# Kernel tuning notes

Hardware: AMD Instinct MI355X
Metric: run time of the kernel (lower is better)

## Reference

```python
import jax, jax.numpy as jnp
import numpy as np


def gcn_conv(x, src, dst, W, b, num_nodes):
    # PyG GCNConv: add self-loops, symmetric deg^-1/2 normalization, scatter-add.
    h = x @ W                                    # [N, out]
    loops = jnp.arange(num_nodes, dtype=src.dtype)
    s = jnp.concatenate([src, loops])            # [E+N]
    d = jnp.concatenate([dst, loops])            # [E+N]
    deg = jax.ops.segment_sum(jnp.ones_like(d, dtype=h.dtype), d, num_segments=num_nodes)
    dinv = jnp.where(deg > 0, jax.lax.rsqrt(deg), 0.0)
    norm = dinv[s] * dinv[d]                     # [E+N]
    msgs = h[s] * norm[:, None]                  # gather + scale  [E+N, out]
    out = jax.ops.segment_sum(msgs, d, num_segments=num_nodes)
    return out + b


NUM_GRAPHS = 512


def setup_inputs() -> dict:
    key = jax.random.key(0)
    ks = jax.random.split(key, 12)
    N, E, F = 50000, 400000, 128
    x = jax.random.normal(ks[0], (N, F), dtype=jnp.float32)
    edge_index = jax.random.randint(ks[1], (2, E), 0, N, dtype=jnp.int64)
    batch = jnp.sort(jax.random.randint(ks[2], (N,), 0, NUM_GRAPHS, dtype=jnp.int64))
    def lin(k, fi, fo):
        return jax.random.normal(k, (fi, fo), dtype=jnp.float32) * (1.0 / np.sqrt(fi))
    return {
        "x": x, "edge_index": edge_index, "batch": batch,
        "W1": lin(ks[3], F, 512), "b1": jnp.zeros((512,), jnp.float32),
        "W2": lin(ks[4], 512, 256), "b2": jnp.zeros((256,), jnp.float32),
        "W3": lin(ks[5], 256, 128), "b3": jnp.zeros((128,), jnp.float32),
        "W4": lin(ks[6], 128, 32), "b4": jnp.zeros((32,), jnp.float32),
        "W5": lin(ks[7], 32, 10), "b5": jnp.zeros((10,), jnp.float32),
    }


def reference(x, edge_index, batch, W1, b1, W2, b2, W3, b3, W4, b4, W5, b5):
    N = x.shape[0]
    src, dst = edge_index[0], edge_index[1]
    h = gcn_conv(x, src, dst, W1, b1, N)
    h = jax.nn.leaky_relu(h, negative_slope=0.01)
    h = gcn_conv(h, src, dst, W2, b2, N)          # [N, 256]
    embs = jax.ops.segment_max(h, batch, num_segments=NUM_GRAPHS)  # [G, 256]
    z = ((h @ W3 + b3) @ W4 + b4) @ W5 + b5       # [N, 10]
    out = jax.ops.segment_max(z, batch, num_segments=NUM_GRAPHS)   # [G, 10]
    return (out, embs)
```

## Files before the change

kernel.cpp:

```cpp
#include <hip/hip_runtime.h>
#include <math.h>

#define DIV_UP(a,b) (((a)+(b)-1)/(b))

typedef __attribute__((ext_vector_type(8))) short bf16x8;
typedef __attribute__((ext_vector_type(4))) float f32x4;

__device__ inline unsigned short f2b(float x) {
    unsigned int u = __float_as_uint(x);
    u += 0x7fffu + ((u >> 16) & 1u);
    return (unsigned short)(u >> 16);
}

__device__ inline void cvt8(uint4 v, float* a) {
    a[0] = __uint_as_float(v.x << 16); a[1] = __uint_as_float(v.x & 0xffff0000u);
    a[2] = __uint_as_float(v.y << 16); a[3] = __uint_as_float(v.y & 0xffff0000u);
    a[4] = __uint_as_float(v.z << 16); a[5] = __uint_as_float(v.z & 0xffff0000u);
    a[6] = __uint_as_float(v.w << 16); a[7] = __uint_as_float(v.w & 0xffff0000u);
}

__device__ inline void gl16(void* lds, const void* g) {
    __builtin_amdgcn_global_load_lds(
        (const __attribute__((address_space(1))) void*)g,
        (__attribute__((address_space(3))) void*)lds, 16, 0, 0);
}

__global__ void k_zero_i(int* p, int n) {
    int i = blockIdx.x * blockDim.x + threadIdx.x;
    if (i < n) p[i] = 0;
}

__global__ void k_hist(const int* __restrict__ dst, int* __restrict__ hist, int E) {
    int i = blockIdx.x * blockDim.x + threadIdx.x;
    if (i < E) atomicAdd(&hist[dst[i]], 1);
}

__global__ __launch_bounds__(256) void k_scan_bsum(const int* __restrict__ hist,
                                                   int* __restrict__ bsum, int N) {
    __shared__ int red[256];
    int t = threadIdx.x;
    int base = blockIdx.x * 1024 + t * 4;
    int s = 0;
    if (base + 3 < N) {
        int4 v = *(const int4*)&hist[base];
        s = v.x + v.y + v.z + v.w;
    } else {
        for (int j = 0; j < 4; ++j) if (base + j < N) s += hist[base + j];
    }
    red[t] = s;
    __syncthreads();
    for (int off = 128; off >= 1; off >>= 1) {
        if (t < off) red[t] += red[t + off];
        __syncthreads();
    }
    if (t == 0) bsum[blockIdx.x] = red[0];
}

__global__ __launch_bounds__(1024) void k_scan_boff(const int* __restrict__ bsum,
        int* __restrict__ boff, int* __restrict__ row_off, int NB, int N) {
    __shared__ int s[1024];
    int t = threadIdx.x;
    int v = (t < NB) ? bsum[t] : 0;
    s[t] = v;
    __syncthreads();
    for (int off = 1; off < 1024; off <<= 1) {
        int u = (t >= off) ? s[t - off] : 0;
        __syncthreads();
        s[t] += u;
        __syncthreads();
    }
    if (t < NB) boff[t] = s[t] - v;
    if (t == NB - 1) row_off[N] = s[t];
}

__global__ __launch_bounds__(256) void k_scan_apply(const int* __restrict__ hist,
        const int* __restrict__ boff, int* __restrict__ row_off,
        float* __restrict__ dinv, int N) {
    __shared__ int s[256];
    int t = threadIdx.x;
    int base = blockIdx.x * 1024 + t * 4;
    int v[4];
    int loc = 0;
#pragma unroll
    for (int j = 0; j < 4; ++j) { v[j] = (base + j < N) ? hist[base + j] : 0; loc += v[j]; }
    s[t] = loc;
    __syncthreads();
    for (int off = 1; off < 256; off <<= 1) {
        int u = (t >= off) ? s[t - off] : 0;
        __syncthreads();
        s[t] += u;
        __syncthreads();
    }
    int run = boff[blockIdx.x] + s[t] - loc;
#pragma unroll
    for (int j = 0; j < 4; ++j) {
        if (base + j < N) {
            row_off[base + j] = run;
            dinv[base + j] = rsqrtf((float)(v[j] + 1));
        }
        run += v[j];
    }
}

__global__ void k_bin(const int* __restrict__ src, const int* __restrict__ dst,
                      const int* __restrict__ row_off, int* __restrict__ cursor,
                      const float* __restrict__ dinv,
                      int* __restrict__ csr_src, float* __restrict__ csr_w, int E) {
    int i = blockIdx.x * blockDim.x + threadIdx.x;
    if (i >= E) return;
    int d = dst[i], s = src[i];
    int pos = row_off[d] + atomicAdd(&cursor[d], 1);
    csr_src[pos] = s;
    csr_w[pos] = dinv[s] * dinv[d];
}

__global__ __launch_bounds__(256) void k_pre(
        const float* __restrict__ W3, const float* __restrict__ W4,
        const float* __restrict__ W5, const float* __restrict__ b3,
        const float* __restrict__ b4, const float* __restrict__ b5,
        float* __restrict__ WcT, float* __restrict__ bc,
        const int* __restrict__ batch, int* __restrict__ bounds, int N, int G, int nb,
        const float* __restrict__ x, unsigned short* __restrict__ xb, int n4,
        const float* __restrict__ W1, unsigned short* __restrict__ w1t, int K1, int N1,
        const float* __restrict__ W2, unsigned short* __restrict__ w2t, int K2, int N2) {
    int b = blockIdx.x;
    int t = threadIdx.x;
    if (b < 11) {
        int c = b;
        if (c < 10) {
            __shared__ float Tc[128];
            if (t < 128) {
                float s = 0.f;
#pragma unroll 8
                for (int k = 0; k < 32; ++k) s = fmaf(W4[t * 32 + k], W5[k * 10 + c], s);
                Tc[t] = s;
            }
            __syncthreads();
            float s = 0.f;
            const float* w3r = &W3[t * 128];
#pragma unroll 8
            for (int j = 0; j < 128; ++j) s = fmaf(w3r[j], Tc[j], s);
            WcT[c * 256 + t] = s;
        } else {
            __shared__ float v[32];
            if (t < 32) {
                float s = b4[t];
                for (int j = 0; j < 128; ++j) s = fmaf(b3[j], W4[j * 32 + t], s);
                v[t] = s;
            }
            __syncthreads();
            if (t < 10) {
                float s = b5[t];
                for (int k = 0; k < 32; ++k) s = fmaf(v[k], W5[k * 10 + t], s);
                bc[t] = s;
            }
        }
        return;
    }
    if (b < 11 + nb) {
        int g = (b - 11) * 256 + t;
        if (g > G) return;
        int lo = 0, hi = N;
        while (lo < hi) { int mid = (lo + hi) >> 1; if (batch[mid] < g) lo = mid + 1; else hi = mid; }
        bounds[g] = lo;
        return;
    }
    int i = (b - 11 - nb) * 256 + t;
    if (i < n4) {
        float4 v = ((const float4*)x)[i];
        ushort4 o;
        o.x = f2b(v.x); o.y = f2b(v.y); o.z = f2b(v.z); o.w = f2b(v.w);
        ((ushort4*)xb)[i] = o;
        return;
    }
    i -= n4;
    if (i < K1 * N1) {
        int k = i / N1, n = i % N1;
        w1t[(size_t)n * K1 + k] = f2b(W1[i]);
        return;
    }
    i -= K1 * N1;
    if (i < K2 * N2) {
        int k = i / N2, n = i % N2;
        w2t[(size_t)n * K2 + k] = f2b(W2[i]);
    }
}

template <int F>
__global__ __launch_bounds__(256) void k_gather_b(const unsigned short* __restrict__ H,
        const int* __restrict__ row_off, const int* __restrict__ csr_src,
        const float* __restrict__ csr_w, const float* __restrict__ dinv,
        const float* __restrict__ bias, unsigned short* __restrict__ outb, int N) {
    const int LPN = F / 8;
    const int NPB = 256 / LPN;
    int node = blockIdx.x * NPB + threadIdx.x / LPN;
    if (node >= N) return;
    int f = (threadIdx.x % LPN) * 8;
    const unsigned short* Hf = H + f;
    float sc = dinv[node]; sc *= sc;
    float a[8];
    cvt8(*(const uint4*)&Hf[(size_t)node * F], a);
#pragma unroll
    for (int j = 0; j < 8; ++j) a[j] *= sc;
    if (bias) {
#pragma unroll
        for (int j = 0; j < 8; ++j) a[j] += bias[f + j];
    }
    int e0 = row_off[node], e1 = row_off[node + 1];
    int e = e0;
    for (; e + 4 <= e1; e += 4) {
        int s0 = csr_src[e + 0], s1 = csr_src[e + 1];
        int s2 = csr_src[e + 2], s3 = csr_src[e + 3];
        uint4 v0 = *(const uint4*)&Hf[(size_t)s0 * F];
        uint4 v1 = *(const uint4*)&Hf[(size_t)s1 * F];
        uint4 v2 = *(const uint4*)&Hf[(size_t)s2 * F];
        uint4 v3 = *(const uint4*)&Hf[(size_t)s3 * F];
        float w0 = csr_w[e + 0], w1 = csr_w[e + 1];
        float w2 = csr_w[e + 2], w3 = csr_w[e + 3];
        float b0[8], b1[8], b2[8], b3[8];
        cvt8(v0, b0); cvt8(v1, b1); cvt8(v2, b2); cvt8(v3, b3);
#pragma unroll
        for (int j = 0; j < 8; ++j) {
            a[j] = fmaf(w0, b0[j], a[j]);
            a[j] = fmaf(w1, b1[j], a[j]);
            a[j] = fmaf(w2, b2[j], a[j]);
            a[j] = fmaf(w3, b3[j], a[j]);
        }
    }
    for (; e < e1; ++e) {
        int s = csr_src[e];
        float w = csr_w[e];
        float b[8];
        cvt8(*(const uint4*)&Hf[(size_t)s * F], b);
#pragma unroll
        for (int j = 0; j < 8; ++j) a[j] = fmaf(w, b[j], a[j]);
    }
    uint4 o;
    o.x = (unsigned)f2b(a[0]) | ((unsigned)f2b(a[1]) << 16);
    o.y = (unsigned)f2b(a[2]) | ((unsigned)f2b(a[3]) << 16);
    o.z = (unsigned)f2b(a[4]) | ((unsigned)f2b(a[5]) << 16);
    o.w = (unsigned)f2b(a[6]) | ((unsigned)f2b(a[7]) << 16);
    *(uint4*)&outb[(size_t)node * F + f] = o;
}

template <int OUT_BF16, int ACT>
__global__ __launch_bounds__(512) void k_gemm_mfma256(const unsigned short* __restrict__ A,
        const unsigned short* __restrict__ Bt, const float* __restrict__ bias,
        void* __restrict__ Cout, int M, int K, int NC) {
    __shared__ __align__(16) unsigned short As[128][64];
    __shared__ __align__(16) unsigned short Bs[256][64];
    int tid = threadIdx.x;
    int wave = tid >> 6, lane = tid & 63;
    int row0 = blockIdx.y * 128, col0 = blockIdx.x * 256;
    int wr = (wave >> 2) * 64, wc = (wave & 3) * 64;
    f32x4 acc[4][4] = {};
    int lr = lane & 15;
    int lg = lane >> 4;
    int sw = ((lane & 7) ^ (lane >> 3)) << 3;
    int ch0 = (lg ^ (lr & 7)) << 3;
    int ch1 = ch0 ^ (4 << 3);

    for (int k0 = 0; k0 < K; k0 += 64) {
#pragma unroll
        for (int c = 0; c < 2; ++c) {
            int rl = c * 64 + wave * 8 + (lane >> 3);
            int gr = min(row0 + rl, M - 1);
            gl16(&As[c * 64 + wave * 8][0], &A[(size_t)gr * K + k0 + sw]);
        }
#pragma unroll
        for (int c = 0; c < 4; ++c) {
            int rl = c * 64 + wave * 8 + (lane >> 3);
            gl16(&Bs[c * 64 + wave * 8][0], &Bt[(size_t)(col0 + rl) * K + k0 + sw]);
        }
        __syncthreads();
        bf16x8 af[2][4], bv[2][4];
#pragma unroll
        for (int i = 0; i < 4; ++i) {
            int ra = wr + i * 16 + lr;
            int rb = wc + i * 16 + lr;
            af[0][i] = *(const bf16x8*)&As[ra][ch0];
            af[1][i] = *(const bf16x8*)&As[ra][ch1];
            bv[0][i] = *(const bf16x8*)&Bs[rb][ch0];
            bv[1][i] = *(const bf16x8*)&Bs[rb][ch1];
        }
#pragma unroll
        for (int s = 0; s < 2; ++s)
#pragma unroll
            for (int i = 0; i < 4; ++i)
#pragma unroll
                for (int j = 0; j < 4; ++j)
                    acc[i][j] = __builtin_amdgcn_mfma_f32_16x16x32_bf16(bv[s][j], af[s][i], acc[i][j], 0, 0, 0);
        __syncthreads();
    }

    int q4 = lg * 4;
    float4 bb[4];
#pragma unroll
    for (int j = 0; j < 4; ++j)
        bb[j] = bias ? *(const float4*)&bias[col0 + wc + j * 16 + q4]
                     : make_float4(0.f, 0.f, 0.f, 0.f);
#pragma unroll
    for (int i = 0; i < 4; ++i) {
        int row = row0 + wr + i * 16 + lr;
        if (row >= M) continue;
#pragma unroll
        for (int j = 0; j < 4; ++j) {
            int c0 = col0 + wc + j * 16 + q4;
            float4 v;
            v.x = acc[i][j][0] + bb[j].x;
            v.y = acc[i][j][1] + bb[j].y;
            v.z = acc[i][j][2] + bb[j].z;
            v.w = acc[i][j][3] + bb[j].w;
            if (ACT) {
                v.x = (v.x >= 0.f) ? v.x : 0.01f * v.x;
                v.y = (v.y >= 0.f) ? v.y : 0.01f * v.y;
                v.z = (v.z >= 0.f) ? v.z : 0.01f * v.z;
                v.w = (v.w >= 0.f) ? v.w : 0.01f * v.w;
            }
            if (OUT_BF16) {
                uint2 o;
                o.x = (unsigned)f2b(v.x) | ((unsigned)f2b(v.y) << 16);
                o.y = (unsigned)f2b(v.z) | ((unsigned)f2b(v.w) << 16);
                *(uint2*)&((unsigned short*)Cout)[(size_t)row * NC + c0] = o;
            } else {
                *(float4*)&((float*)Cout)[(size_t)row * NC + c0] = v;
            }
        }
    }
}

__global__ __launch_bounds__(320) void k_head_segmax(const unsigned short* __restrict__ H,
        const float* __restrict__ WcT, const float* __restrict__ bc,
        const int* __restrict__ bounds, float* __restrict__ out,
        float* __restrict__ out_emb) {
    __shared__ __align__(16) float Ws[10][260];
    __shared__ float bs[10];
    __shared__ float red[320];
    int t = threadIdx.x;
    for (int i = t; i < 2560; i += 320) Ws[i / 256][i % 256] = WcT[i];
    if (t < 10) bs[t] = bc[t];
    __syncthreads();
    int g = blockIdx.x;
    int s = bounds[g], e = bounds[g + 1];
    int col = t % 10, rs = t / 10;
    float m = -INFINITY;
    for (int r = s + rs; r < e; r += 32) {
        const unsigned short* hr = &H[(size_t)r * 256];
        float acc = bs[col];
#pragma unroll 4
        for (int k = 0; k < 256; k += 8) {
            float h[8];
            cvt8(*(const uint4*)&hr[k], h);
            float4 wa = *(const float4*)&Ws[col][k];
            float4 wb = *(const float4*)&Ws[col][k + 4];
            acc = fmaf(h[0], wa.x, acc);
            acc = fmaf(h[1], wa.y, acc);
            acc = fmaf(h[2], wa.z, acc);
            acc = fmaf(h[3], wa.w, acc);
            acc = fmaf(h[4], wb.x, acc);
            acc = fmaf(h[5], wb.y, acc);
            acc = fmaf(h[6], wb.z, acc);
            acc = fmaf(h[7], wb.w, acc);
        }
        m = fmaxf(m, acc);
    }
    red[t] = m;
    __syncthreads();
    for (int step = 16; step >= 1; step >>= 1) {
        if (rs < step) red[rs * 10 + col] = fmaxf(red[rs * 10 + col], red[(rs + step) * 10 + col]);
        __syncthreads();
    }
    if (rs == 0) out[(size_t)g * 10 + col] = red[col];
    if (t < 256) {
        float mm = -INFINITY;
        for (int r = s; r < e; ++r)
            mm = fmaxf(mm, __uint_as_float(((unsigned)H[(size_t)r * 256 + t]) << 16));
        out_emb[(size_t)g * 256 + t] = mm;
    }
}

extern "C" void kernel_launch(void* const* d_in, const int* in_sizes, int n_in,
                              void* d_out, int out_size, void* d_ws, size_t ws_size,
                              hipStream_t stream) {
    const float* x  = (const float*)d_in[0];
    const int* ei   = (const int*)d_in[1];
    const int* batch= (const int*)d_in[2];
    const float* W1 = (const float*)d_in[3];
    const float* b1 = (const float*)d_in[4];
    const float* W2 = (const float*)d_in[5];
    const float* b2 = (const float*)d_in[6];
    const float* W3 = (const float*)d_in[7];
    const float* b3 = (const float*)d_in[8];
    const float* W4 = (const float*)d_in[9];
    const float* b4 = (const float*)d_in[10];
    const float* W5 = (const float*)d_in[11];
    const float* b5 = (const float*)d_in[12];

    const int N  = in_sizes[2];
    const int F  = in_sizes[0] / N;
    const int E  = in_sizes[1] / 2;
    const int C1 = in_sizes[4];
    const int C2 = in_sizes[6];
    const int C5 = in_sizes[12];
    const int G  = out_size / (C2 + C5);
    const int NB = DIV_UP(N, 1024);

    const int* srcp = ei;
    const int* dstp = ei + E;

    uintptr_t p = (uintptr_t)d_ws;
    auto carve = [&](size_t bytes) {
        uintptr_t r = p;
        p += (bytes + 255) & ~(size_t)255;
        return (void*)r;
    };
    int* hist    = (int*)carve(sizeof(int) * N);
    int* cursor  = (int*)carve(sizeof(int) * N);
    int* row_off = (int*)carve(sizeof(int) * (N + 1));
    int* bounds  = (int*)carve(sizeof(int) * (G + 1));
    int* bsum    = (int*)carve(sizeof(int) * NB);
    int* boff    = (int*)carve(sizeof(int) * NB);
    int* csr_src = (int*)carve(sizeof(int) * E);
    float* csr_w = (float*)carve(sizeof(float) * E);
    float* dinv  = (float*)carve(sizeof(float) * N);
    float* wct   = (float*)carve(sizeof(float) * C2 * C5);
    float* bcv   = (float*)carve(sizeof(float) * C5);
    unsigned short* w1t = (unsigned short*)carve(sizeof(short) * F * C1);
    unsigned short* w2t = (unsigned short*)carve(sizeof(short) * C1 * C2);
    unsigned short* xb    = (unsigned short*)carve(sizeof(short) * (size_t)N * F);
    unsigned short* aggxb = (unsigned short*)carve(sizeof(short) * (size_t)N * F);
    unsigned short* h1b   = (unsigned short*)carve(sizeof(short) * (size_t)N * C1);
    unsigned short* t2b   = (unsigned short*)carve(sizeof(short) * (size_t)N * C2);
    unsigned short* h2b   = (unsigned short*)carve(sizeof(short) * (size_t)N * C2);

    float* out     = (float*)d_out;
    float* out_emb = out + (size_t)G * C5;

    int zspan = (int)(((sizeof(int) * N + 255) & ~(size_t)255) / 4) + N;
    k_zero_i<<<DIV_UP(zspan, 256), 256, 0, stream>>>(hist, zspan);
    k_hist<<<DIV_UP(E, 256), 256, 0, stream>>>(dstp, hist, E);
    k_scan_bsum<<<NB, 256, 0, stream>>>(hist, bsum, N);
    k_scan_boff<<<1, 1024, 0, stream>>>(bsum, boff, row_off, NB, N);
    k_scan_apply<<<NB, 256, 0, stream>>>(hist, boff, row_off, dinv, N);
    k_bin<<<DIV_UP(E, 256), 256, 0, stream>>>(srcp, dstp, row_off, cursor, dinv,
                                              csr_src, csr_w, E);

    int n4 = N * F / 4;
    int nb_bounds = DIV_UP(G + 1, 256);
    int prep_total = n4 + F * C1 + C1 * C2;
    int pre_blocks = 11 + nb_bounds + DIV_UP(prep_total, 256);
    k_pre<<<pre_blocks, 256, 0, stream>>>(W3, W4, W5, b3, b4, b5, wct, bcv,
                                          batch, bounds, N, G, nb_bounds,
                                          x, xb, n4, W1, w1t, F, C1, W2, w2t, C1, C2);

    k_gather_b<128><<<DIV_UP(N, 16), 256, 0, stream>>>(
        xb, row_off, csr_src, csr_w, dinv, nullptr, aggxb, N);
    dim3 g1(C1 / 256, DIV_UP(N, 128));
    k_gemm_mfma256<1, 1><<<g1, 512, 0, stream>>>(aggxb, w1t, b1, h1b, N, F, C1);

    dim3 g2(C2 / 256, DIV_UP(N, 128));
    k_gemm_mfma256<1, 0><<<g2, 512, 0, stream>>>(h1b, w2t, nullptr, t2b, N, C1, C2);
    k_gather_b<256><<<DIV_UP(N, 8), 256, 0, stream>>>(
        t2b, row_off, csr_src, csr_w, dinv, b2, h2b, N);

    k_head_segmax<<<G, 320, 0, stream>>>(h2b, wct, bcv, bounds, out, out_emb);
}
```

Measured before the change: 286.4 us.

## Fuse CSR build and preprocessing into one cooperative grid-synced kernel

Replaces the zero, histogram, three-pass scan, binning and preprocessing launches with a single cooperative kernel that separates the phases with grid-wide syncs, removing several launch gaps and small-kernel tails. The gather kernel also gains an 8-edge unrolled loop so more neighbor-row loads are in flight at once. The risks are grid.sync costs, a fixed 256x1024 grid that may not suit every phase, and higher register pressure in the gather.

```diff
diff --git a/kernel.cpp b/kernel.cpp
--- a/kernel.cpp
+++ b/kernel.cpp
@@ -1,5 +1,8 @@
 #include <hip/hip_runtime.h>
+#include <hip/hip_cooperative_groups.h>
 #include <math.h>
+
+namespace cg = cooperative_groups;
 
 #define DIV_UP(a,b) (((a)+(b)-1)/(b))
 
@@ -25,164 +28,139 @@
         (__attribute__((address_space(3))) void*)lds, 16, 0, 0);
 }
 
-__global__ void k_zero_i(int* p, int n) {
-    int i = blockIdx.x * blockDim.x + threadIdx.x;
-    if (i < n) p[i] = 0;
-}
-
-__global__ void k_hist(const int* __restrict__ dst, int* __restrict__ hist, int E) {
-    int i = blockIdx.x * blockDim.x + threadIdx.x;
-    if (i < E) atomicAdd(&hist[dst[i]], 1);
-}
-
-__global__ __launch_bounds__(256) void k_scan_bsum(const int* __restrict__ hist,
-                                                   int* __restrict__ bsum, int N) {
-    __shared__ int red[256];
-    int t = threadIdx.x;
-    int base = blockIdx.x * 1024 + t * 4;
-    int s = 0;
-    if (base + 3 < N) {
-        int4 v = *(const int4*)&hist[base];
-        s = v.x + v.y + v.z + v.w;
-    } else {
-        for (int j = 0; j < 4; ++j) if (base + j < N) s += hist[base + j];
-    }
-    red[t] = s;
-    __syncthreads();
-    for (int off = 128; off >= 1; off >>= 1) {
-        if (t < off) red[t] += red[t + off];
-        __syncthreads();
-    }
-    if (t == 0) bsum[blockIdx.x] = red[0];
-}
-
-__global__ __launch_bounds__(1024) void k_scan_boff(const int* __restrict__ bsum,
-        int* __restrict__ boff, int* __restrict__ row_off, int NB, int N) {
-    __shared__ int s[1024];
-    int t = threadIdx.x;
-    int v = (t < NB) ? bsum[t] : 0;
-    s[t] = v;
-    __syncthreads();
-    for (int off = 1; off < 1024; off <<= 1) {
-        int u = (t >= off) ? s[t - off] : 0;
-        __syncthreads();
-        s[t] += u;
-        __syncthreads();
-    }
-    if (t < NB) boff[t] = s[t] - v;
-    if (t == NB - 1) row_off[N] = s[t];
-}
-
-__global__ __launch_bounds__(256) void k_scan_apply(const int* __restrict__ hist,
-        const int* __restrict__ boff, int* __restrict__ row_off,
-        float* __restrict__ dinv, int N) {
-    __shared__ int s[256];
-    int t = threadIdx.x;
-    int base = blockIdx.x * 1024 + t * 4;
-    int v[4];
-    int loc = 0;
-#pragma unroll
-    for (int j = 0; j < 4; ++j) { v[j] = (base + j < N) ? hist[base + j] : 0; loc += v[j]; }
-    s[t] = loc;
-    __syncthreads();
-    for (int off = 1; off < 256; off <<= 1) {
-        int u = (t >= off) ? s[t - off] : 0;
-        __syncthreads();
-        s[t] += u;
-        __syncthreads();
-    }
-    int run = boff[blockIdx.x] + s[t] - loc;
-#pragma unroll
-    for (int j = 0; j < 4; ++j) {
-        if (base + j < N) {
-            row_off[base + j] = run;
-            dinv[base + j] = rsqrtf((float)(v[j] + 1));
-        }
-        run += v[j];
-    }
-}
-
-__global__ void k_bin(const int* __restrict__ src, const int* __restrict__ dst,
-                      const int* __restrict__ row_off, int* __restrict__ cursor,
-                      const float* __restrict__ dinv,
-                      int* __restrict__ csr_src, float* __restrict__ csr_w, int E) {
-    int i = blockIdx.x * blockDim.x + threadIdx.x;
-    if (i >= E) return;
-    int d = dst[i], s = src[i];
-    int pos = row_off[d] + atomicAdd(&cursor[d], 1);
-    csr_src[pos] = s;
-    csr_w[pos] = dinv[s] * dinv[d];
-}
-
-__global__ __launch_bounds__(256) void k_pre(
+__global__ __launch_bounds__(1024) void k_build(
+        const int* __restrict__ src, const int* __restrict__ dst, int E,
+        int* __restrict__ hist, int* __restrict__ cursor, int* __restrict__ bsum,
+        int* __restrict__ row_off, float* __restrict__ dinv, int N,
+        int* __restrict__ csr_src, float* __restrict__ csr_w,
+        const int* __restrict__ batch, int* __restrict__ bounds, int G,
         const float* __restrict__ W3, const float* __restrict__ W4,
         const float* __restrict__ W5, const float* __restrict__ b3,
         const float* __restrict__ b4, const float* __restrict__ b5,
         float* __restrict__ WcT, float* __restrict__ bc,
-        const int* __restrict__ batch, int* __restrict__ bounds, int N, int G, int nb,
         const float* __restrict__ x, unsigned short* __restrict__ xb, int n4,
         const float* __restrict__ W1, unsigned short* __restrict__ w1t, int K1, int N1,
         const float* __restrict__ W2, unsigned short* __restrict__ w2t, int K2, int N2) {
-    int b = blockIdx.x;
-    int t = threadIdx.x;
-    if (b < 11) {
-        int c = b;
-        if (c < 10) {
-            __shared__ float Tc[128];
-            if (t < 128) {
-                float s = 0.f;
-#pragma unroll 8
-                for (int k = 0; k < 32; ++k) s = fmaf(W4[t * 32 + k], W5[k * 10 + c], s);
-                Tc[t] = s;
-            }
-            __syncthreads();
-            float s = 0.f;
-            const float* w3r = &W3[t * 128];
-#pragma unroll 8
-            for (int j = 0; j < 128; ++j) s = fmaf(w3r[j], Tc[j], s);
-            WcT[c * 256 + t] = s;
-        } else {
-            __shared__ float v[32];
-            if (t < 32) {
-                float s = b4[t];
-                for (int j = 0; j < 128; ++j) s = fmaf(b3[j], W4[j * 32 + t], s);
-                v[t] = s;
-            }
-            __syncthreads();
-            if (t < 10) {
-                float s = b5[t];
-                for (int k = 0; k < 32; ++k) s = fmaf(v[k], W5[k * 10 + t], s);
-                bc[t] = s;
-            }
-        }
-        return;
-    }
-    if (b < 11 + nb) {
-        int g = (b - 11) * 256 + t;
-        if (g > G) return;
-        int lo = 0, hi = N;
-        while (lo < hi) { int mid = (lo + hi) >> 1; if (batch[mid] < g) lo = mid + 1; else hi = mid; }
-        bounds[g] = lo;
-        return;
-    }
-    int i = (b - 11 - nb) * 256 + t;
-    if (i < n4) {
+    cg::grid_group grid = cg::this_grid();
+    __shared__ float shf[256];
+    __shared__ int ssc[1024];
+    const int nb = gridDim.x;
+    const int b = blockIdx.x, t = threadIdx.x;
+    const int gtid = b * blockDim.x + t;
+    const int gsz = nb * blockDim.x;
+
+    for (int i = gtid; i < N; i += gsz) { hist[i] = 0; cursor[i] = 0; }
+    for (int i = gtid; i < n4; i += gsz) {
         float4 v = ((const float4*)x)[i];
         ushort4 o;
         o.x = f2b(v.x); o.y = f2b(v.y); o.z = f2b(v.z); o.w = f2b(v.w);
         ((ushort4*)xb)[i] = o;
-        return;
-    }
-    i -= n4;
-    if (i < K1 * N1) {
+    }
+    for (int i = gtid; i < K1 * N1; i += gsz) {
         int k = i / N1, n = i % N1;
         w1t[(size_t)n * K1 + k] = f2b(W1[i]);
-        return;
-    }
-    i -= K1 * N1;
-    if (i < K2 * N2) {
+    }
+    for (int i = gtid; i < K2 * N2; i += gsz) {
         int k = i / N2, n = i % N2;
         w2t[(size_t)n * K2 + k] = f2b(W2[i]);
+    }
+    for (int g = gtid; g <= G; g += gsz) {
+        int lo = 0, hi = N;
+        while (lo < hi) { int mid = (lo + hi) >> 1; if (batch[mid] < g) lo = mid + 1; else hi = mid; }
+        bounds[g] = lo;
+    }
+    if (b < 10) {
+        int c = b;
+        if (t < 128) {
+            float s = 0.f;
+#pragma unroll 8
+            for (int k = 0; k < 32; ++k) s = fmaf(W4[t * 32 + k], W5[k * 10 + c], s);
+            shf[t] = s;
+        }
+        __syncthreads();
+        if (t < 256) {
+            float s = 0.f;
+            const float* w3r = &W3[t * 128];
+#pragma unroll 8
+            for (int j = 0; j < 128; ++j) s = fmaf(w3r[j], shf[j], s);
+            WcT[c * 256 + t] = s;
+        }
+        __syncthreads();
+    } else if (b == 10) {
+        if (t < 32) {
+            float s = b4[t];
+            for (int j = 0; j < 128; ++j) s = fmaf(b3[j], W4[j * 32 + t], s);
+            shf[t] = s;
+        }
+        __syncthreads();
+        if (t < 10) {
+            float s = b5[t];
+            for (int k = 0; k < 32; ++k) s = fmaf(shf[k], W5[k * 10 + t], s);
+            bc[t] = s;
+        }
+        __syncthreads();
+    }
+    grid.sync();
+
+    for (int i = gtid; i < E; i += gsz) atomicAdd(&hist[dst[i]], 1);
+    grid.sync();
+
+    const int chunk = DIV_UP(N, nb);
+    const int beg = b * chunk;
+    const int end = min(beg + chunk, N);
+    {
+        int s = 0;
+        for (int i = beg + t; i < end; i += 1024) s += hist[i];
+        ssc[t] = s;
+        __syncthreads();
+        for (int off = 512; off >= 1; off >>= 1) {
+            if (t < off) ssc[t] += ssc[t + off];
+            __syncthreads();
+        }
+        if (t == 0) bsum[b] = ssc[0];
+    }
+    grid.sync();
+
+    {
+        int v = (t < nb) ? bsum[t] : 0;
+        ssc[t] = v;
+        __syncthreads();
+        for (int off = 1; off < 1024; off <<= 1) {
+            int u = (t >= off) ? ssc[t - off] : 0;
+            __syncthreads();
+            ssc[t] += u;
+            __syncthreads();
+        }
+        int boffv = (b == 0) ? 0 : ssc[b - 1];
+        __syncthreads();
+        int carry = boffv;
+        for (int s0 = beg; s0 < end; s0 += 1024) {
+            int i = s0 + t;
+            int v2 = (i < end) ? hist[i] : 0;
+            ssc[t] = v2;
+            __syncthreads();
+            for (int off = 1; off < 1024; off <<= 1) {
+                int u = (t >= off) ? ssc[t - off] : 0;
+                __syncthreads();
+                ssc[t] += u;
+                __syncthreads();
+            }
+            if (i < end) {
+                row_off[i] = carry + ssc[t] - v2;
+                dinv[i] = rsqrtf((float)(v2 + 1));
+            }
+            carry += ssc[1023];
+            __syncthreads();
+        }
+        if (b == nb - 1 && t == 0) row_off[N] = carry;
+    }
+    grid.sync();
+
+    for (int i = gtid; i < E; i += gsz) {
+        int d = dst[i], s = src[i];
+        int pos = row_off[d] + atomicAdd(&cursor[d], 1);
+        csr_src[pos] = s;
+        csr_w[pos] = dinv[s] * dinv[d];
     }
 }
 
@@ -208,6 +186,24 @@
     }
     int e0 = row_off[node], e1 = row_off[node + 1];
     int e = e0;
+    for (; e + 8 <= e1; e += 8) {
+        int ss[8];
+        uint4 vv[8];
+        float ww[8];
+#pragma unroll
+        for (int q = 0; q < 8; ++q) ss[q] = csr_src[e + q];
+#pragma unroll
+        for (int q = 0; q < 8; ++q) vv[q] = *(const uint4*)&Hf[(size_t)ss[q] * F];
+#pragma unroll
+        for (int q = 0; q < 8; ++q) ww[q] = csr_w[e + q];
+#pragma unroll
+        for (int q = 0; q < 8; ++q) {
+            float bb[8];
+            cvt8(vv[q], bb);
+#pragma unroll
+            for (int j = 0; j < 8; ++j) a[j] = fmaf(ww[q], bb[j], a[j]);
+        }
+    }
     for (; e + 4 <= e1; e += 4) {
         int s0 = csr_src[e + 0], s1 = csr_src[e + 1];
         int s2 = csr_src[e + 2], s3 = csr_src[e + 3];
@@ -398,12 +394,11 @@
 
     const int N  = in_sizes[2];
     const int F  = in_sizes[0] / N;
-    const int E  = in_sizes[1] / 2;
+    int E        = in_sizes[1] / 2;
     const int C1 = in_sizes[4];
     const int C2 = in_sizes[6];
     const int C5 = in_sizes[12];
     const int G  = out_size / (C2 + C5);
-    const int NB = DIV_UP(N, 1024);
 
     const int* srcp = ei;
     const int* dstp = ei + E;
@@ -418,8 +413,7 @@
     int* cursor  = (int*)carve(sizeof(int) * N);
     int* row_off = (int*)carve(sizeof(int) * (N + 1));
     int* bounds  = (int*)carve(sizeof(int) * (G + 1));
-    int* bsum    = (int*)carve(sizeof(int) * NB);
-    int* boff    = (int*)carve(sizeof(int) * NB);
+    int* bsum    = (int*)carve(sizeof(int) * 256);
     int* csr_src = (int*)carve(sizeof(int) * E);
     float* csr_w = (float*)carve(sizeof(float) * E);
     float* dinv  = (float*)carve(sizeof(float) * N);
@@ -436,22 +430,21 @@
     float* out     = (float*)d_out;
     float* out_emb = out + (size_t)G * C5;
 
-    int zspan = (int)(((sizeof(int) * N + 255) & ~(size_t)255) / 4) + N;
-    k_zero_i<<<DIV_UP(zspan, 256), 256, 0, stream>>>(hist, zspan);
-    k_hist<<<DIV_UP(E, 256), 256, 0, stream>>>(dstp, hist, E);
-    k_scan_bsum<<<NB, 256, 0, stream>>>(hist, bsum, N);
-    k_scan_boff<<<1, 1024, 0, stream>>>(bsum, boff, row_off, NB, N);
-    k_scan_apply<<<NB, 256, 0, stream>>>(hist, boff, row_off, dinv, N);
-    k_bin<<<DIV_UP(E, 256), 256, 0, stream>>>(srcp, dstp, row_off, cursor, dinv,
-                                              csr_src, csr_w, E);
-
     int n4 = N * F / 4;
-    int nb_bounds = DIV_UP(G + 1, 256);
-    int prep_total = n4 + F * C1 + C1 * C2;
-    int pre_blocks = 11 + nb_bounds + DIV_UP(prep_total, 256);
-    k_pre<<<pre_blocks, 256, 0, stream>>>(W3, W4, W5, b3, b4, b5, wct, bcv,
-                                          batch, bounds, N, G, nb_bounds,
-                                          x, xb, n4, W1, w1t, F, C1, W2, w2t, C1, C2);
+    int K1 = F, N1 = C1, K2 = C1, N2v = C2;
+    int Nv = N, Gv = G, Ev = E;
+    void* cargs[] = {
+        (void*)&srcp, (void*)&dstp, (void*)&Ev,
+        (void*)&hist, (void*)&cursor, (void*)&bsum,
+        (void*)&row_off, (void*)&dinv, (void*)&Nv,
+        (void*)&csr_src, (void*)&csr_w,
+        (void*)&batch, (void*)&bounds, (void*)&Gv,
+        (void*)&W3, (void*)&W4, (void*)&W5, (void*)&b3, (void*)&b4, (void*)&b5,
+        (void*)&wct, (void*)&bcv,
+        (void*)&x, (void*)&xb, (void*)&n4,
+        (void*)&W1, (void*)&w1t, (void*)&K1, (void*)&N1,
+        (void*)&W2, (void*)&w2t, (void*)&K2, (void*)&N2v };
+    hipLaunchCooperativeKernel((void*)k_build, dim3(256), dim3(1024), cargs, 0, stream);
 
     k_gather_b<128><<<DIV_UP(N, 16), 256, 0, stream>>>(
         xb, row_off, csr_src, csr_w, dinv, nullptr, aggxb, N);
```

After: 438.7 us. 1.53x slower.
